# Kernel tuning notes

Measured on AMD Instinct MI355X. Metric: run time of the kernel, lower is better.

Reference implementation:

```python
import jax, jax.numpy as jnp
import numpy as np

B, C, H, W = 8, 128, 64, 64  # dim = in_channels = 128, N = H*W = 4096
TEMP = float(C) ** 0.5


def _proj(x, w, b):
    # 1x1 conv: [B,C,H,W] x [D,C] -> [B,D,H,W]
    return jnp.einsum('bchw,dc->bdhw', x, w) + b[None, :, None, None]


def setup_inputs() -> dict:
    key = jax.random.key(0)
    ks = jax.random.split(key, 6)
    std = 0.01
    x = jax.random.normal(ks[0], (B, C, H, W), dtype=jnp.float32)
    wq = jax.random.normal(ks[1], (C, C), dtype=jnp.float32) * std
    wk = jax.random.normal(ks[2], (C, C), dtype=jnp.float32) * std
    wv = jax.random.normal(ks[3], (C, C), dtype=jnp.float32) * std
    wo = jax.random.normal(ks[4], (C, C), dtype=jnp.float32) * std
    zeros = jnp.zeros((C,), dtype=jnp.float32)
    return {"x": x, "wq": wq, "bq": zeros, "wk": wk, "bk": zeros,
            "wv": wv, "bv": zeros, "wo": wo, "bo": zeros}


def reference(x, wq, bq, wk, bk, wv, bv, wo, bo):
    n, c, h, w = x.shape
    N = h * w
    q = _proj(x, wq, bq).reshape(n, c, N)          # [B, D, N]
    k = _proj(x, wk, bk).reshape(n, c, N)          # [B, D, N]
    v = _proj(x, wv, bv).reshape(n, c, N)          # [B, D, N]
    # attn[b, i, j] = sum_d q[b,d,i] * k[b,d,j] / temp
    attn = jnp.einsum('bdi,bdj->bij', q, k) / TEMP  # [B, N, N]
    attn = jax.nn.softmax(attn, axis=-1)
    # y[b, d, i] = sum_j attn[b,i,j] * v[b,d,j]
    y = jnp.einsum('bij,bdj->bdi', attn, v).reshape(n, c, h, w)
    y = _proj(y, wo, bo)                            # conv_out
    return x + y                                    # identity residual
```

## Files before the change

### kernel.cpp

```cpp
#include <hip/hip_runtime.h>


typedef float  f32x4  __attribute__((ext_vector_type(4)));
typedef float  f32x16 __attribute__((ext_vector_type(16)));
typedef short  s16x8  __attribute__((ext_vector_type(8)));
typedef short  s16x4  __attribute__((ext_vector_type(4)));
typedef unsigned uint4v __attribute__((ext_vector_type(4)));

#define MFMA16(A, Bb, Cc) __builtin_amdgcn_mfma_f32_16x16x32_bf16(A, Bb, Cc, 0, 0, 0)
#define MFMA32(A, Bb, Cc) __builtin_amdgcn_mfma_f32_32x32x16_bf16(A, Bb, Cc, 0, 0, 0)

#define BATCH 8
#define DIM   128
#define NN    4096
#define NSPLIT 2
#define JCHUNK (NN / NSPLIT)
#define Q_SCALE 0.12751649736784776f

__device__ __forceinline__ unsigned short f2bf(float f) {
  union { float f; unsigned u; } v; v.f = f;
  unsigned r = v.u + 0x7FFFu + ((v.u >> 16) & 1u);
  return (unsigned short)(r >> 16);
}
__device__ __forceinline__ float bf2f(unsigned short h) {
  union { unsigned u; float f; } v; v.u = ((unsigned)h) << 16;
  return v.f;
}
__device__ __forceinline__ s16x8 cvt8(const float* src) {
  float4 a = *(const float4*)src;
  float4 b = *(const float4*)(src + 4);
  s16x8 f;
  f[0] = (short)f2bf(a.x); f[1] = (short)f2bf(a.y);
  f[2] = (short)f2bf(a.z); f[3] = (short)f2bf(a.w);
  f[4] = (short)f2bf(b.x); f[5] = (short)f2bf(b.y);
  f[6] = (short)f2bf(b.z); f[7] = (short)f2bf(b.w);
  return f;
}

__global__ __launch_bounds__(256) void qkv_kernel(
    const float* __restrict__ x,
    const float* __restrict__ wq, const float* __restrict__ wk,
    const float* __restrict__ wv,
    const float* __restrict__ bq, const float* __restrict__ bk,
    const float* __restrict__ bv,
    unsigned short* __restrict__ qt,
    unsigned short* __restrict__ kt,
    unsigned short* __restrict__ vv) {
  __shared__ float xs[DIM * 68];
  __shared__ unsigned short wls[DIM * 136];
  const int b = blockIdx.y;
  const int i0 = blockIdx.x * 64;
  const int tid = threadIdx.x;

  for (int idx = tid; idx < 2048; idx += 256) {
    int c = idx >> 4, i4 = idx & 15;
    float4 val = *(const float4*)(x + ((size_t)(b * DIM + c)) * NN + i0 + i4 * 4);
    xs[c * 68 + i4 * 4 + 0] = val.x;
    xs[c * 68 + i4 * 4 + 1] = val.y;
    xs[c * 68 + i4 * 4 + 2] = val.z;
    xs[c * 68 + i4 * 4 + 3] = val.w;
  }
  __syncthreads();

  const int w = tid >> 6, lane = tid & 63, quad = lane >> 4, l15 = lane & 15;
  const int iloc = w * 16 + l15;

  s16x8 bfrag[4];
#pragma unroll
  for (int ch = 0; ch < 4; ch++) {
    s16x8 f;
#pragma unroll
    for (int jj = 0; jj < 8; jj++) {
      int c = ch * 32 + quad * 8 + jj;
      f[jj] = (short)f2bf(xs[c * 68 + iloc]);
    }
    bfrag[ch] = f;
  }

  const int i = i0 + iloc;
  const int wr = tid >> 4, wc = tid & 15;

  for (int z = 0; z < 3; z++) {
    __syncthreads();
    const float* wsrc = (z == 0) ? wq : (z == 1) ? wk : wv;
#pragma unroll
    for (int it = 0; it < 8; it++) {
      const int row = it * 16 + wr;
      *(s16x8*)(&wls[row * 136 + wc * 8]) = cvt8(wsrc + row * DIM + wc * 8);
    }
    __syncthreads();

    const float* bias = (z == 0) ? bq : (z == 1) ? bk : bv;
    const float sc = (z == 0) ? Q_SCALE : 1.0f;

    for (int t = 0; t < 8; t++) {
      const int dl = t * 16;
      f32x4 acc = {0.f, 0.f, 0.f, 0.f};
#pragma unroll
      for (int ch = 0; ch < 4; ch++) {
        s16x8 af = *(const s16x8*)(&wls[(dl + l15) * 136 + ch * 32 + quad * 8]);
        acc = MFMA16(af, bfrag[ch], acc);
      }
      if (z < 2) {
        unsigned short* dstb = (z == 0) ? qt : kt;
        s16x4 o;
#pragma unroll
        for (int r = 0; r < 4; r++) {
          int d = dl + quad * 4 + r;
          o[r] = (short)f2bf((acc[r] + bias[d]) * sc);
        }
        *(s16x4*)(dstb + ((size_t)b * NN + i) * DIM + dl + quad * 4) = o;
      } else {
#pragma unroll
        for (int r = 0; r < 4; r++) {
          int d = dl + quad * 4 + r;
          vv[((size_t)b * DIM + d) * NN + i] = f2bf(acc[r] + bias[d]);
        }
      }
    }
  }
}

__global__ __launch_bounds__(256, 2) void attn_kernel(
    const unsigned short* __restrict__ qt,
    const unsigned short* __restrict__ kt,
    const unsigned short* __restrict__ vv,
    unsigned short* __restrict__ o_part,
    float* __restrict__ l_part) {
  __shared__ unsigned short sh[16384];
  const int b = blockIdx.y;
  const int i0 = blockIdx.x * 128;
  const int split = blockIdx.z;
  const int jbase = split * JCHUNK;
  const int tid = threadIdx.x;
  const int w = tid >> 6, lane = tid & 63;
  const int l31 = lane & 31, h = lane >> 5;

  const unsigned short* kb = kt + (size_t)b * NN * DIM;
  const unsigned short* vb = vv + (size_t)b * DIM * NN;

  s16x8 qfrag[8];
  {
    const unsigned short* qrow =
        qt + ((size_t)b * NN + i0 + w * 32 + l31) * DIM + h * 8;
#pragma unroll
    for (int kc = 0; kc < 8; kc++)
      qfrag[kc] = *(const s16x8*)(qrow + kc * 16);
  }

  f32x16 acc[4];
#pragma unroll
  for (int mt = 0; mt < 4; mt++)
#pragma unroll
    for (int e = 0; e < 16; e++) acc[mt][e] = 0.f;
  float l_acc = 0.f;

  const int kr = tid >> 4, kc_ = tid & 15;
  const int vr = tid >> 3, vc = tid & 7;
  const int vch0 = (vc & 1) ? (vc - 1) : vc;
  const int vch1 = (vc & 1) ? vc : (vc + 1);
  const int vpos = (vc & 1) * 4;

  s16x8 kpre[4], vpre[4];
#pragma unroll
  for (int it = 0; it < 4; it++) {
    kpre[it] = *(const s16x8*)(kb + (size_t)(jbase + it * 16 + kr) * DIM + kc_ * 8);
    vpre[it] = *(const s16x8*)(vb + (size_t)(it * 32 + vr) * NN + jbase + vc * 8);
  }

  for (int j0 = jbase; j0 < jbase + JCHUNK; j0 += 64) {
    __syncthreads();
#pragma unroll
    for (int it = 0; it < 4; it++) {
      const int r = it * 16 + kr;
      *(s16x8*)(sh + (((r << 4) + (kc_ ^ (r & 15))) << 3)) = kpre[it];
      const int r2 = it * 32 + vr;
      union { s16x8 v8; s16x4 v4[2]; } sp; sp.v8 = vpre[it];
      *(s16x4*)(sh + 8192 + (((r2 << 3) + (vch0 ^ (r2 & 7))) << 3) + vpos) = sp.v4[0];
      *(s16x4*)(sh + 8192 + (((r2 << 3) + (vch1 ^ (r2 & 7))) << 3) + vpos) = sp.v4[1];
    }
    __syncthreads();

    if (j0 + 64 < jbase + JCHUNK) {
      const int jn = j0 + 64;
#pragma unroll
      for (int it = 0; it < 4; it++) {
        kpre[it] = *(const s16x8*)(kb + (size_t)(jn + it * 16 + kr) * DIM + kc_ * 8);
        vpre[it] = *(const s16x8*)(vb + (size_t)(it * 32 + vr) * NN + jn + vc * 8);
      }
    }

#pragma unroll
    for (int jt = 0; jt < 2; jt++) {
      f32x16 S;
#pragma unroll
      for (int e = 0; e < 16; e++) S[e] = 0.f;
      const int j = jt * 32 + l31;
#pragma unroll
      for (int kc = 0; kc < 8; kc++) {
        s16x8 kf = *(const s16x8*)(sh + (((j << 4) + ((2 * kc + h) ^ (j & 15))) << 3));
        S = MFMA32(kf, qfrag[kc], S);
      }
      unsigned pk[8];
#pragma unroll
      for (int p = 0; p < 8; p++) {
        float e0 = exp2f(S[2 * p]), e1 = exp2f(S[2 * p + 1]);
        l_acc += e0 + e1;
        union { float f; unsigned u; } u0, u1; u0.f = e0; u1.f = e1;
        pk[p] = __builtin_amdgcn_perm(u1.u, u0.u, 0x07060302u);
      }
#pragma unroll
      for (int bl = 0; bl < 2; bl++) {
        union { uint4v u; s16x8 v; } pu;
        pu.u[0] = pk[4 * bl + 0]; pu.u[1] = pk[4 * bl + 1];
        pu.u[2] = pk[4 * bl + 2]; pu.u[3] = pk[4 * bl + 3];
        const s16x8 pf = pu.v;
        const int c0 = (jt * 2 + bl) * 2 + h;
#pragma unroll
        for (int mt = 0; mt < 4; mt++) {
          const int d = mt * 32 + l31;
          s16x8 vf = *(const s16x8*)(sh + 8192 + (((d << 3) + (c0 ^ (d & 7))) << 3));
          acc[mt] = MFMA32(vf, pf, acc[mt]);
        }
      }
    }
  }

  const float l_tot = l_acc + __shfl_xor(l_acc, 32, 64);

  __syncthreads();
  unsigned short* ep = sh + w * 4096;
#pragma unroll
  for (int mt = 0; mt < 4; mt++)
#pragma unroll
    for (int reg = 0; reg < 16; reg++) {
      int d = mt * 32 + (reg & 3) + 8 * (reg >> 2) + 4 * h;
      int dc = d >> 3;
      ep[(l31 << 7) + ((dc ^ (l31 & 15)) << 3) + (d & 7)] = f2bf(acc[mt][reg]);
    }
  __syncthreads();
#pragma unroll
  for (int it = 0; it < 8; it++) {
    int qr = it * 4 + (lane >> 4), cr = lane & 15;
    s16x8 v = *(const s16x8*)(ep + (qr << 7) + ((cr ^ (qr & 15)) << 3));
    *(s16x8*)(o_part + (((size_t)split * BATCH + b) * NN + i0 + w * 32 + qr) * DIM +
              cr * 8) = v;
  }
  if (lane < 32)
    l_part[((size_t)split * BATCH + b) * NN + i0 + w * 32 + lane] = l_tot;
}

__global__ __launch_bounds__(256) void outp_kernel(
    const float* __restrict__ x,
    const float* __restrict__ wo,
    const float* __restrict__ bo,
    const unsigned short* __restrict__ o_part,
    const float* __restrict__ l_part,
    float* __restrict__ out) {
  __shared__ unsigned short ytile[64 * 136];
  __shared__ unsigned short wls[DIM * 136];
  __shared__ float invl[64];
  const int b = blockIdx.y;
  const int i0 = blockIdx.x * 64;
  const int tid = threadIdx.x;
  const int wr = tid >> 4, wc = tid & 15;

#pragma unroll
  for (int it = 0; it < 8; it++) {
    const int row = it * 16 + wr;
    *(s16x8*)(&wls[row * 136 + wc * 8]) = cvt8(wo + row * DIM + wc * 8);
  }

  if (tid < 64) {
    float l = 0.f;
#pragma unroll
    for (int s = 0; s < NSPLIT; s++)
      l += l_part[((size_t)s * BATCH + b) * NN + i0 + tid];
    invl[tid] = 1.0f / l;
  }
  __syncthreads();

#pragma unroll
  for (int k = 0; k < 4; k++) {
    int slot = k * 256 + tid;
    int i = slot >> 4, g = slot & 15;
    float o[8] = {0.f, 0.f, 0.f, 0.f, 0.f, 0.f, 0.f, 0.f};
#pragma unroll
    for (int s = 0; s < NSPLIT; s++) {
      s16x8 ov = *(const s16x8*)(o_part +
                                 (((size_t)s * BATCH + b) * NN + i0 + i) * DIM + g * 8);
#pragma unroll
      for (int jj = 0; jj < 8; jj++) o[jj] += bf2f((unsigned short)ov[jj]);
    }
    const float inv = invl[i];
    s16x8 f;
#pragma unroll
    for (int jj = 0; jj < 8; jj++) f[jj] = (short)f2bf(o[jj] * inv);
    *(s16x8*)(&ytile[i * 136 + g * 8]) = f;
  }
  __syncthreads();

  const int w = tid >> 6, lane = tid & 63, quad = lane >> 4, l15 = lane & 15;
  const int i = i0 + w * 16 + l15;

  s16x8 bfrag[4];
#pragma unroll
  for (int ch = 0; ch < 4; ch++)
    bfrag[ch] = *(const s16x8*)(&ytile[(w * 16 + l15) * 136 + ch * 32 + quad * 8]);

  for (int t = 0; t < 8; t++) {
    f32x4 acc = {0.f, 0.f, 0.f, 0.f};
#pragma unroll
    for (int ch = 0; ch < 4; ch++) {
      s16x8 af = *(const s16x8*)(&wls[(t * 16 + l15) * 136 + ch * 32 + quad * 8]);
      acc = MFMA16(af, bfrag[ch], acc);
    }
#pragma unroll
    for (int r = 0; r < 4; r++) {
      int d = t * 16 + quad * 4 + r;
      size_t idx = ((size_t)b * DIM + d) * NN + i;
      out[idx] = x[idx] + acc[r] + bo[d];
    }
  }
}

extern "C" void kernel_launch(void* const* d_in, const int* in_sizes, int n_in,
                              void* d_out, int out_size, void* d_ws, size_t ws_size,
                              hipStream_t stream) {
  const float* x  = (const float*)d_in[0];
  const float* wq = (const float*)d_in[1];
  const float* bq = (const float*)d_in[2];
  const float* wk = (const float*)d_in[3];
  const float* bk = (const float*)d_in[4];
  const float* wv = (const float*)d_in[5];
  const float* bv = (const float*)d_in[6];
  const float* wo = (const float*)d_in[7];
  const float* bo = (const float*)d_in[8];
  float* out = (float*)d_out;

  unsigned short* ws  = (unsigned short*)d_ws;
  unsigned short* qt  = ws;
  unsigned short* kt  = qt + (size_t)BATCH * NN * DIM;
  unsigned short* vv  = kt + (size_t)BATCH * NN * DIM;
  unsigned short* o_part = vv + (size_t)BATCH * NN * DIM;
  float* l_part = (float*)(o_part + (size_t)NSPLIT * BATCH * NN * DIM);

  hipLaunchKernelGGL(qkv_kernel, dim3(64, 8), dim3(256), 0, stream,
                     x, wq, wk, wv, bq, bk, bv, qt, kt, vv);
  hipLaunchKernelGGL(attn_kernel, dim3(32, 8, NSPLIT), dim3(256), 0, stream,
                     qt, kt, vv, o_part, l_part);
  hipLaunchKernelGGL(outp_kernel, dim3(64, 8), dim3(256), 0, stream,
                     x, wo, bo, o_part, l_part, out);
}
```

Measured before the change: 178.3 us.

## Double-buffer K/V tiles in LDS with one barrier per step and raw exp2

The attention inner loop now keeps two LDS buffers for K/V tiles. The next tile is written to the alternate buffer while the current one is consumed, which drops one __syncthreads per iteration, and global prefetch runs two tiles ahead. The change also brackets the MFMA sections with s_setprio and uses the hardware exp2 builtin instead of libm exp2f. LDS use doubles to 64KB per block, which may limit occupancy under launch_bounds(256,2).

New measurement: 174.0 us (median of 2 runs). 2.4% less time.

```diff
diff --git a/kernel.cpp b/kernel.cpp
--- a/kernel.cpp
+++ b/kernel.cpp
@@ -15,7 +15,14 @@
 #define NN    4096
 #define NSPLIT 2
 #define JCHUNK (NN / NSPLIT)
+#define NT    (JCHUNK / 64)
 #define Q_SCALE 0.12751649736784776f
+
+#if __has_builtin(__builtin_amdgcn_exp2f)
+#define EXP2(x) __builtin_amdgcn_exp2f(x)
+#else
+#define EXP2(x) exp2f(x)
+#endif
 
 __device__ __forceinline__ unsigned short f2bf(float f) {
   union { float f; unsigned u; } v; v.f = f;
@@ -127,7 +134,7 @@
     const unsigned short* __restrict__ vv,
     unsigned short* __restrict__ o_part,
     float* __restrict__ l_part) {
-  __shared__ unsigned short sh[16384];
+  __shared__ unsigned short sh[32768];
   const int b = blockIdx.y;
   const int i0 = blockIdx.x * 128;
   const int split = blockIdx.z;
@@ -162,27 +169,45 @@
   const int vpos = (vc & 1) * 4;
 
   s16x8 kpre[4], vpre[4];
+
 #pragma unroll
   for (int it = 0; it < 4; it++) {
     kpre[it] = *(const s16x8*)(kb + (size_t)(jbase + it * 16 + kr) * DIM + kc_ * 8);
     vpre[it] = *(const s16x8*)(vb + (size_t)(it * 32 + vr) * NN + jbase + vc * 8);
   }
-
-  for (int j0 = jbase; j0 < jbase + JCHUNK; j0 += 64) {
+#pragma unroll
+  for (int it = 0; it < 4; it++) {
+    const int r = it * 16 + kr;
+    *(s16x8*)(sh + (((r << 4) + (kc_ ^ (r & 15))) << 3)) = kpre[it];
+    const int r2 = it * 32 + vr;
+    union { s16x8 v8; s16x4 v4[2]; } sp; sp.v8 = vpre[it];
+    *(s16x4*)(sh + 8192 + (((r2 << 3) + (vch0 ^ (r2 & 7))) << 3) + vpos) = sp.v4[0];
+    *(s16x4*)(sh + 8192 + (((r2 << 3) + (vch1 ^ (r2 & 7))) << 3) + vpos) = sp.v4[1];
+  }
+#pragma unroll
+  for (int it = 0; it < 4; it++) {
+    kpre[it] = *(const s16x8*)(kb + (size_t)(jbase + 64 + it * 16 + kr) * DIM + kc_ * 8);
+    vpre[it] = *(const s16x8*)(vb + (size_t)(it * 32 + vr) * NN + jbase + 64 + vc * 8);
+  }
+
+  for (int t = 0; t < NT; t++) {
     __syncthreads();
-#pragma unroll
-    for (int it = 0; it < 4; it++) {
-      const int r = it * 16 + kr;
-      *(s16x8*)(sh + (((r << 4) + (kc_ ^ (r & 15))) << 3)) = kpre[it];
-      const int r2 = it * 32 + vr;
-      union { s16x8 v8; s16x4 v4[2]; } sp; sp.v8 = vpre[it];
-      *(s16x4*)(sh + 8192 + (((r2 << 3) + (vch0 ^ (r2 & 7))) << 3) + vpos) = sp.v4[0];
-      *(s16x4*)(sh + 8192 + (((r2 << 3) + (vch1 ^ (r2 & 7))) << 3) + vpos) = sp.v4[1];
-    }
-    __syncthreads();
-
-    if (j0 + 64 < jbase + JCHUNK) {
-      const int jn = j0 + 64;
+
+    if (t + 1 < NT) {
+      unsigned short* wb = sh + ((~t & 1) << 14);
+#pragma unroll
+      for (int it = 0; it < 4; it++) {
+        const int r = it * 16 + kr;
+        *(s16x8*)(wb + (((r << 4) + (kc_ ^ (r & 15))) << 3)) = kpre[it];
+        const int r2 = it * 32 + vr;
+        union { s16x8 v8; s16x4 v4[2]; } sp; sp.v8 = vpre[it];
+        *(s16x4*)(wb + 8192 + (((r2 << 3) + (vch0 ^ (r2 & 7))) << 3) + vpos) = sp.v4[0];
+        *(s16x4*)(wb + 8192 + (((r2 << 3) + (vch1 ^ (r2 & 7))) << 3) + vpos) = sp.v4[1];
+      }
+    }
+
+    if (t + 2 < NT) {
+      const int jn = jbase + (t + 2) * 64;
 #pragma unroll
       for (int it = 0; it < 4; it++) {
         kpre[it] = *(const s16x8*)(kb + (size_t)(jn + it * 16 + kr) * DIM + kc_ * 8);
@@ -190,25 +215,31 @@
       }
     }
 
+    const unsigned short* rK = sh + ((t & 1) << 14);
+    const unsigned short* rV = rK + 8192;
+
 #pragma unroll
     for (int jt = 0; jt < 2; jt++) {
       f32x16 S;
 #pragma unroll
       for (int e = 0; e < 16; e++) S[e] = 0.f;
       const int j = jt * 32 + l31;
+      __builtin_amdgcn_s_setprio(1);
 #pragma unroll
       for (int kc = 0; kc < 8; kc++) {
-        s16x8 kf = *(const s16x8*)(sh + (((j << 4) + ((2 * kc + h) ^ (j & 15))) << 3));
+        s16x8 kf = *(const s16x8*)(rK + (((j << 4) + ((2 * kc + h) ^ (j & 15))) << 3));
         S = MFMA32(kf, qfrag[kc], S);
       }
+      __builtin_amdgcn_s_setprio(0);
       unsigned pk[8];
 #pragma unroll
       for (int p = 0; p < 8; p++) {
-        float e0 = exp2f(S[2 * p]), e1 = exp2f(S[2 * p + 1]);
+        float e0 = EXP2(S[2 * p]), e1 = EXP2(S[2 * p + 1]);
         l_acc += e0 + e1;
         union { float f; unsigned u; } u0, u1; u0.f = e0; u1.f = e1;
         pk[p] = __builtin_amdgcn_perm(u1.u, u0.u, 0x07060302u);
       }
+      __builtin_amdgcn_s_setprio(1);
 #pragma unroll
       for (int bl = 0; bl < 2; bl++) {
         union { uint4v u; s16x8 v; } pu;
@@ -219,10 +250,11 @@
 #pragma unroll
         for (int mt = 0; mt < 4; mt++) {
           const int d = mt * 32 + l31;
-          s16x8 vf = *(const s16x8*)(sh + 8192 + (((d << 3) + (c0 ^ (d & 7))) << 3));
+          s16x8 vf = *(const s16x8*)(rV + (((d << 3) + (c0 ^ (d & 7))) << 3));
           acc[mt] = MFMA32(vf, pf, acc[mt]);
         }
       }
+      __builtin_amdgcn_s_setprio(0);
     }
   }
 
```
